# Performance work log

Measured on AMD Instinct MI355X. Metric: run time of the kernel, lower is better.

The kernel has to match this reference:

```python
import jax, jax.numpy as jnp
import numpy as np

B, V = 256, 2048
PD, MD, H = 1024, 512, 512

def setup_inputs() -> dict:
    key = jax.random.key(0)
    k1, k2, k3, k4, k5 = jax.random.split(key, 5)
    patient_emb = jax.random.normal(k1, (B, PD), dtype=jnp.float32)
    atc4_emb = jax.random.normal(k2, (V, MD), dtype=jnp.float32)
    # Linear(PD+MD -> H): weight (H, PD+MD), bias (H,)
    W1 = jax.random.normal(k3, (H, PD + MD), dtype=jnp.float32) * 0.02
    b1 = jnp.zeros((H,), dtype=jnp.float32)
    # Linear(H -> 1): weight (1, H) -> store as (H,), bias scalar
    w2 = jax.random.normal(k4, (H,), dtype=jnp.float32) * 0.05
    b2 = jnp.zeros((), dtype=jnp.float32)
    return {"patient_emb": patient_emb, "atc4_emb": atc4_emb,
            "W1": W1, "b1": b1, "w2": w2, "b2": b2}

def reference(patient_emb, atc4_emb, W1, b1, w2, b2):
    # Algebraically equivalent to cat([patient, mol]) @ W1.T:
    # split W1 into patient and mol blocks, matmul each, broadcast-add.
    W1p = W1[:, :PD]   # (H, PD)
    W1m = W1[:, PD:]   # (H, MD)
    hp = jnp.einsum('bp,hp->bh', patient_emb, W1p)   # (B, H)
    hm = jnp.einsum('vm,hm->vh', atc4_emb, W1m)      # (V, H)
    h = jnp.tanh(hp[:, None, :] + hm[None, :, :] + b1)  # (B, V, H)
    scores = jnp.einsum('bvh,h->bv', h, w2) + b2     # (B, V)
    return scores
```

## Files before the change

kernel.cpp:

```cpp
#include <hip/hip_runtime.h>
#include <hip/hip_bf16.h>
#include <math.h>

typedef __attribute__((ext_vector_type(8))) short short8;
typedef __attribute__((ext_vector_type(4))) float float4v;
typedef __attribute__((ext_vector_type(2))) float float2v;

__device__ __forceinline__ float2v lo2(float4v v) {
    return __builtin_shufflevector(v, v, 0, 1);
}
__device__ __forceinline__ float2v hi2(float4v v) {
    return __builtin_shufflevector(v, v, 2, 3);
}

__device__ __forceinline__ int2 cvt2bf16x4(float4v v) {
    union { __hip_bfloat162 h2; int i; } u0, u1;
    u0.h2 = __float22bfloat162_rn(make_float2(v.x, v.y));
    u1.h2 = __float22bfloat162_rn(make_float2(v.z, v.w));
    return make_int2(u0.i, u1.i);
}

__global__ __launch_bounds__(256, 2) void gemm_exp(
    const float* __restrict__ patient, const float* __restrict__ atc4,
    const float* __restrict__ W1, const float* __restrict__ b1,
    float* __restrict__ EA, float* __restrict__ EM)
{
    const float* A; const float* W; const float* bias; float* T;
    int lda, K, M;
    int bx = blockIdx.x;
    if (bx < 4) {
        A = patient; lda = 1024; K = 1024; M = 256; bias = b1; T = EA; W = W1;
    } else {
        bx -= 4;
        A = atc4;    lda = 512;  K = 512;  M = 2048; bias = nullptr; T = EM; W = W1 + 1024;
    }
    const int ldw = 1536;

    __shared__ short As[64][72];
    __shared__ short Bs[64][72];
    const int t = threadIdx.x;
    const int m0 = bx * 64;
    const int n0 = blockIdx.y * 64;
    const int wave = t >> 6;
    const int lane = t & 63;
    const int wm = (wave & 1) * 32;
    const int wn = (wave >> 1) * 32;
    const int lrow = lane & 15;
    const int quad = lane >> 4;

    float4v acc[2][2];
    #pragma unroll
    for (int i = 0; i < 2; i++)
        #pragma unroll
        for (int j = 0; j < 2; j++)
            acc[i][j] = (float4v){0.f, 0.f, 0.f, 0.f};

    const int sr = t >> 2;
    const int sc = (t & 3) * 16;

    float4v av[4], wv[4];
    {
        const float* ap = A + (size_t)(m0 + sr) * lda + sc;
        const float* wp = W + (size_t)(n0 + sr) * ldw + sc;
        #pragma unroll
        for (int ii = 0; ii < 4; ii++) {
            av[ii] = *(const float4v*)(ap + ii * 4);
            wv[ii] = *(const float4v*)(wp + ii * 4);
        }
    }

    for (int k0 = 0; k0 < K; k0 += 64) {
        #pragma unroll
        for (int ii = 0; ii < 4; ii++) {
            *(int2*)&As[sr][sc + ii * 4] = cvt2bf16x4(av[ii]);
            *(int2*)&Bs[sr][sc + ii * 4] = cvt2bf16x4(wv[ii]);
        }
        __syncthreads();
        if (k0 + 64 < K) {
            const float* ap = A + (size_t)(m0 + sr) * lda + (k0 + 64 + sc);
            const float* wp = W + (size_t)(n0 + sr) * ldw + (k0 + 64 + sc);
            #pragma unroll
            for (int ii = 0; ii < 4; ii++) {
                av[ii] = *(const float4v*)(ap + ii * 4);
                wv[ii] = *(const float4v*)(wp + ii * 4);
            }
        }
        #pragma unroll
        for (int kk = 0; kk < 64; kk += 32) {
            short8 af[2], bfr[2];
            #pragma unroll
            for (int i = 0; i < 2; i++)
                af[i] = *(const short8*)&As[wm + i * 16 + lrow][kk + quad * 8];
            #pragma unroll
            for (int j = 0; j < 2; j++)
                bfr[j] = *(const short8*)&Bs[wn + j * 16 + lrow][kk + quad * 8];
            #pragma unroll
            for (int i = 0; i < 2; i++)
                #pragma unroll
                for (int j = 0; j < 2; j++)
                    acc[i][j] = __builtin_amdgcn_mfma_f32_16x16x32_bf16(
                        af[i], bfr[j], acc[i][j], 0, 0, 0);
        }
        __syncthreads();
    }

    #pragma unroll
    for (int i = 0; i < 2; i++) {
        #pragma unroll
        for (int j = 0; j < 2; j++) {
            const int n  = n0 + wn + j * 16 + lrow;
            const int mb = m0 + wm + i * 16 + quad * 4;
            const float bn = bias ? bias[n] : 0.0f;
            float4v ev;
            #pragma unroll
            for (int r = 0; r < 4; r++)
                ev[r] = __expf(2.0f * (acc[i][j][r] + bn));
            *(float4v*)&T[(size_t)n * M + mb] = ev;
        }
    }
}

__device__ __forceinline__ void rat4(
    float2v em0, float2v em1, float2v em2, float2v em3,
    float2v a0, float2v a1, float2v a2, float2v a3,
    float2v c0, float2v c1, float2v c2, float2v c3,
    float2v& acc)
{
    const float2v one2 = {1.f, 1.f};
    float2v d0 = __builtin_elementwise_fma(em0, a0, one2);
    float2v d1 = __builtin_elementwise_fma(em1, a1, one2);
    float2v d2 = __builtin_elementwise_fma(em2, a2, one2);
    float2v d3 = __builtin_elementwise_fma(em3, a3, one2);
    float2v e01 = d0 * d1;
    float2v e23 = d2 * d3;
    float2v n01 = __builtin_elementwise_fma(d1, c0, d0 * c1);
    float2v n23 = __builtin_elementwise_fma(d3, c2, d2 * c3);
    float2v num = __builtin_elementwise_fma(n01, e23, n23 * e01);
    float2v den = e01 * e23;
    float2v r = { __builtin_amdgcn_rcpf(den.x), __builtin_amdgcn_rcpf(den.y) };
    acc = __builtin_elementwise_fma(num, r, acc);
}

__global__ __launch_bounds__(256, 4) void pair_kernel(
    const float* __restrict__ EA, const float* __restrict__ EM,
    const float* __restrict__ w2, float* __restrict__ partial)
{
    __shared__ float sEA[64][68];
    __shared__ float sEM[64][68];
    __shared__ float4v sC4[16];
    const int t  = threadIdx.x;
    const int v0 = blockIdx.x * 64;
    const int b0 = blockIdx.y * 64;
    const int h0 = blockIdx.z * 64;
    const int tx = t & 15;
    const int ty = t >> 4;

    if (t < 16) {
        float4v wvq = *(const float4v*)(w2 + h0 + 4 * t);
        sC4[t] = -2.0f * wvq;
    }

    float2v accL[4], accH[4];
    #pragma unroll
    for (int i = 0; i < 4; i++) {
        accL[i] = (float2v){0.f, 0.f};
        accH[i] = (float2v){0.f, 0.f};
    }

    {
        const int rS = t >> 2;
        const int c0i = (t & 3) * 16;
        const float* pa = EA + (size_t)(h0 + rS) * 256 + b0 + c0i;
        const float* pm = EM + (size_t)(h0 + rS) * 2048 + v0 + c0i;
        #pragma unroll
        for (int i = 0; i < 4; i++) {
            float4v va = *(const float4v*)(pa + 4 * i);
            float4v vm = *(const float4v*)(pm + 4 * i);
            *(float4v*)&sEA[rS][c0i + 4 * i] = va;
            *(float4v*)&sEM[rS][c0i + 4 * i] = vm;
        }
    }
    __syncthreads();

    #pragma unroll 1
    for (int q = 0; q < 16; q++) {
        const int hq = 4 * q;
        const float4v m0 = *(const float4v*)&sEM[hq    ][tx * 4];
        const float4v m1 = *(const float4v*)&sEM[hq + 1][tx * 4];
        const float4v m2 = *(const float4v*)&sEM[hq + 2][tx * 4];
        const float4v m3 = *(const float4v*)&sEM[hq + 3][tx * 4];
        const float4v ea0 = *(const float4v*)&sEA[hq    ][ty * 4];
        const float4v ea1 = *(const float4v*)&sEA[hq + 1][ty * 4];
        const float4v ea2 = *(const float4v*)&sEA[hq + 2][ty * 4];
        const float4v ea3 = *(const float4v*)&sEA[hq + 3][ty * 4];
        const float4v c = sC4[q];
        const float2v c0 = { c.x, c.x };
        const float2v c1 = { c.y, c.y };
        const float2v c2 = { c.z, c.z };
        const float2v c3 = { c.w, c.w };
        const float2v m0L = lo2(m0), m0H = hi2(m0);
        const float2v m1L = lo2(m1), m1H = hi2(m1);
        const float2v m2L = lo2(m2), m2H = hi2(m2);
        const float2v m3L = lo2(m3), m3H = hi2(m3);
        #pragma unroll
        for (int i = 0; i < 4; i++) {
            const float2v a0 = { ea0[i], ea0[i] };
            const float2v a1 = { ea1[i], ea1[i] };
            const float2v a2 = { ea2[i], ea2[i] };
            const float2v a3 = { ea3[i], ea3[i] };
            rat4(m0L, m1L, m2L, m3L, a0, a1, a2, a3, c0, c1, c2, c3, accL[i]);
            rat4(m0H, m1H, m2H, m3H, a0, a1, a2, a3, c0, c1, c2, c3, accH[i]);
        }
    }

    float4v w2q = sC4[0];
    #pragma unroll
    for (int k = 1; k < 16; k++) w2q += sC4[k];
    const float w2s = -0.5f * (w2q.x + w2q.y + w2q.z + w2q.w);

    const size_t pb = (size_t)blockIdx.z * (256 * 2048);
    #pragma unroll
    for (int i = 0; i < 4; i++) {
        const size_t row = pb + (size_t)(b0 + ty * 4 + i) * 2048 + v0 + tx * 4;
        float4v o = { accL[i].x + w2s, accL[i].y + w2s,
                      accH[i].x + w2s, accH[i].y + w2s };
        *(float4v*)&partial[row] = o;
    }
}

__global__ __launch_bounds__(256) void reduce_kernel(
    const float* __restrict__ partial, const float* __restrict__ b2,
    float* __restrict__ out)
{
    const int i = (blockIdx.x * 256 + threadIdx.x) * 4;
    const float bb = b2[0];
    float4v s = *(const float4v*)&partial[i];
    #pragma unroll
    for (int z = 1; z < 8; z++)
        s += *(const float4v*)&partial[(size_t)z * 524288 + i];
    float4v o = s + bb;
    *(float4v*)&out[i] = o;
}

extern "C" void kernel_launch(void* const* d_in, const int* in_sizes, int n_in,
                              void* d_out, int out_size, void* d_ws, size_t ws_size,
                              hipStream_t stream)
{
    const float* patient = (const float*)d_in[0];
    const float* atc4    = (const float*)d_in[1];
    const float* W1      = (const float*)d_in[2];
    const float* b1      = (const float*)d_in[3];
    const float* w2      = (const float*)d_in[4];
    const float* b2      = (const float*)d_in[5];
    float* out = (float*)d_out;
    float* ws  = (float*)d_ws;

    float* EA      = ws;
    float* EM      = ws + 131072;
    float* partial = ws + 1179648;

    gemm_exp<<<dim3(36, 8, 1), 256, 0, stream>>>(patient, atc4, W1, b1, EA, EM);
    pair_kernel<<<dim3(32, 4, 8), 256, 0, stream>>>(EA, EM, w2, partial);
    reduce_kernel<<<512, 256, 0, stream>>>(partial, b2, out);
}
```

Baseline: 110.8 us.

## Enlarge GEMM M-tile to 128 and double-buffer LDS with single barrier

The projection GEMM now uses 128x64 tiles per block, with each wave computing a 64x32 sub-tile, which halves the grid to 18x8 blocks. Shared memory is double-buffered so the next tile's bf16 conversion and store overlap with the current MFMA work, leaving one barrier per k-step instead of two. The goal is better operand reuse and less synchronisation. The cost is more registers and LDS per block (launch bounds drop to 1) and only 144 blocks, which may underfill the GPU's compute units.

```diff
diff --git a/kernel.cpp b/kernel.cpp
--- a/kernel.cpp
+++ b/kernel.cpp
@@ -20,7 +20,7 @@
     return make_int2(u0.i, u1.i);
 }
 
-__global__ __launch_bounds__(256, 2) void gemm_exp(
+__global__ __launch_bounds__(256, 1) void gemm_exp(
     const float* __restrict__ patient, const float* __restrict__ atc4,
     const float* __restrict__ W1, const float* __restrict__ b1,
     float* __restrict__ EA, float* __restrict__ EM)
@@ -28,84 +28,97 @@
     const float* A; const float* W; const float* bias; float* T;
     int lda, K, M;
     int bx = blockIdx.x;
-    if (bx < 4) {
+    if (bx < 2) {
         A = patient; lda = 1024; K = 1024; M = 256; bias = b1; T = EA; W = W1;
     } else {
-        bx -= 4;
+        bx -= 2;
         A = atc4;    lda = 512;  K = 512;  M = 2048; bias = nullptr; T = EM; W = W1 + 1024;
     }
     const int ldw = 1536;
 
-    __shared__ short As[64][72];
-    __shared__ short Bs[64][72];
+    __shared__ short As[2][128][72];
+    __shared__ short Bs[2][64][72];
     const int t = threadIdx.x;
-    const int m0 = bx * 64;
+    const int m0 = bx * 128;
     const int n0 = blockIdx.y * 64;
     const int wave = t >> 6;
     const int lane = t & 63;
-    const int wm = (wave & 1) * 32;
+    const int wm = (wave & 1) * 64;
     const int wn = (wave >> 1) * 32;
     const int lrow = lane & 15;
     const int quad = lane >> 4;
 
-    float4v acc[2][2];
-    #pragma unroll
-    for (int i = 0; i < 2; i++)
+    float4v acc[4][2];
+    #pragma unroll
+    for (int i = 0; i < 4; i++)
         #pragma unroll
         for (int j = 0; j < 2; j++)
             acc[i][j] = (float4v){0.f, 0.f, 0.f, 0.f};
 
-    const int sr = t >> 2;
-    const int sc = (t & 3) * 16;
-
-    float4v av[4], wv[4];
+    const int sa_r = t >> 1;
+    const int sa_c = (t & 1) * 32;
+    const int sb_r = t >> 2;
+    const int sb_c = (t & 3) * 16;
+
+    float4v av[8], wv[4];
     {
-        const float* ap = A + (size_t)(m0 + sr) * lda + sc;
-        const float* wp = W + (size_t)(n0 + sr) * ldw + sc;
-        #pragma unroll
-        for (int ii = 0; ii < 4; ii++) {
-            av[ii] = *(const float4v*)(ap + ii * 4);
-            wv[ii] = *(const float4v*)(wp + ii * 4);
-        }
-    }
-
+        const float* ap = A + (size_t)(m0 + sa_r) * lda + sa_c;
+        #pragma unroll
+        for (int ii = 0; ii < 8; ii++) av[ii] = *(const float4v*)(ap + ii * 4);
+        const float* wp = W + (size_t)(n0 + sb_r) * ldw + sb_c;
+        #pragma unroll
+        for (int ii = 0; ii < 4; ii++) wv[ii] = *(const float4v*)(wp + ii * 4);
+        #pragma unroll
+        for (int ii = 0; ii < 8; ii++)
+            *(int2*)&As[0][sa_r][sa_c + ii * 4] = cvt2bf16x4(av[ii]);
+        #pragma unroll
+        for (int ii = 0; ii < 4; ii++)
+            *(int2*)&Bs[0][sb_r][sb_c + ii * 4] = cvt2bf16x4(wv[ii]);
+    }
+    __syncthreads();
+
+    int cur = 0;
     for (int k0 = 0; k0 < K; k0 += 64) {
-        #pragma unroll
-        for (int ii = 0; ii < 4; ii++) {
-            *(int2*)&As[sr][sc + ii * 4] = cvt2bf16x4(av[ii]);
-            *(int2*)&Bs[sr][sc + ii * 4] = cvt2bf16x4(wv[ii]);
-        }
-        __syncthreads();
-        if (k0 + 64 < K) {
-            const float* ap = A + (size_t)(m0 + sr) * lda + (k0 + 64 + sc);
-            const float* wp = W + (size_t)(n0 + sr) * ldw + (k0 + 64 + sc);
-            #pragma unroll
-            for (int ii = 0; ii < 4; ii++) {
-                av[ii] = *(const float4v*)(ap + ii * 4);
-                wv[ii] = *(const float4v*)(wp + ii * 4);
-            }
+        const bool has_next = (k0 + 64 < K);
+        if (has_next) {
+            const float* ap = A + (size_t)(m0 + sa_r) * lda + (k0 + 64 + sa_c);
+            #pragma unroll
+            for (int ii = 0; ii < 8; ii++) av[ii] = *(const float4v*)(ap + ii * 4);
+            const float* wp = W + (size_t)(n0 + sb_r) * ldw + (k0 + 64 + sb_c);
+            #pragma unroll
+            for (int ii = 0; ii < 4; ii++) wv[ii] = *(const float4v*)(wp + ii * 4);
         }
         #pragma unroll
         for (int kk = 0; kk < 64; kk += 32) {
-            short8 af[2], bfr[2];
-            #pragma unroll
-            for (int i = 0; i < 2; i++)
-                af[i] = *(const short8*)&As[wm + i * 16 + lrow][kk + quad * 8];
+            short8 af[4], bfr[2];
+            #pragma unroll
+            for (int i = 0; i < 4; i++)
+                af[i] = *(const short8*)&As[cur][wm + i * 16 + lrow][kk + quad * 8];
             #pragma unroll
             for (int j = 0; j < 2; j++)
-                bfr[j] = *(const short8*)&Bs[wn + j * 16 + lrow][kk + quad * 8];
-            #pragma unroll
-            for (int i = 0; i < 2; i++)
+                bfr[j] = *(const short8*)&Bs[cur][wn + j * 16 + lrow][kk + quad * 8];
+            #pragma unroll
+            for (int i = 0; i < 4; i++)
                 #pragma unroll
                 for (int j = 0; j < 2; j++)
                     acc[i][j] = __builtin_amdgcn_mfma_f32_16x16x32_bf16(
                         af[i], bfr[j], acc[i][j], 0, 0, 0);
         }
-        __syncthreads();
-    }
-
-    #pragma unroll
-    for (int i = 0; i < 2; i++) {
+        if (has_next) {
+            const int nxt = cur ^ 1;
+            #pragma unroll
+            for (int ii = 0; ii < 8; ii++)
+                *(int2*)&As[nxt][sa_r][sa_c + ii * 4] = cvt2bf16x4(av[ii]);
+            #pragma unroll
+            for (int ii = 0; ii < 4; ii++)
+                *(int2*)&Bs[nxt][sb_r][sb_c + ii * 4] = cvt2bf16x4(wv[ii]);
+            __syncthreads();
+            cur = nxt;
+        }
+    }
+
+    #pragma unroll
+    for (int i = 0; i < 4; i++) {
         #pragma unroll
         for (int j = 0; j < 2; j++) {
             const int n  = n0 + wn + j * 16 + lrow;
@@ -259,7 +272,7 @@
     float* EM      = ws + 131072;
     float* partial = ws + 1179648;
 
-    gemm_exp<<<dim3(36, 8, 1), 256, 0, stream>>>(patient, atc4, W1, b1, EA, EM);
+    gemm_exp<<<dim3(18, 8, 1), 256, 0, stream>>>(patient, atc4, W1, b1, EA, EM);
     pair_kernel<<<dim3(32, 4, 8), 256, 0, stream>>>(EA, EM, w2, partial);
     reduce_kernel<<<512, 256, 0, stream>>>(partial, b2, out);
 }
```

Result: slower. 124.7 us (+12.5%).
